# Kernel optimization log

Measured on AMD Instinct MI355X. Metric: run time of the kernel, lower is better.

Reference implementation:

```python
import jax, jax.numpy as jnp
import numpy as np

B, C, H, W = 4, 256, 48, 48
NUM_HEADS = 8
INTER = C // 2          # squeeze_ratio = 2
HEAD_DIM = INTER // NUM_HEADS


def setup_inputs() -> dict:
    key = jax.random.key(0)
    ks = jax.random.split(key, 11)
    s_in = 1.0 / np.sqrt(C)      # torch Conv2d default init scale (uniform bound)
    s_mid = 1.0 / np.sqrt(INTER)
    return {
        "rgb":   jax.random.normal(ks[0], (B, C, H, W), jnp.float32),
        "depth": jax.random.normal(ks[1], (B, C, H, W), jnp.float32),
        "rgbd":  jax.random.normal(ks[2], (B, C, H, W), jnp.float32),
        # 1x1 convs == channel matmuls; store as [out, in] plus bias
        "Wq": jax.random.uniform(ks[3], (INTER, C), jnp.float32, -s_in, s_in),
        "bq": jax.random.uniform(ks[4], (INTER,), jnp.float32, -s_in, s_in),
        "Wk": jax.random.uniform(ks[5], (INTER, C), jnp.float32, -s_in, s_in),
        "bk": jax.random.uniform(ks[6], (INTER,), jnp.float32, -s_in, s_in),
        "Wv": jax.random.uniform(ks[7], (INTER, C), jnp.float32, -s_in, s_in),
        "bv": jax.random.uniform(ks[8], (INTER,), jnp.float32, -s_in, s_in),
        "Wo": jax.random.uniform(ks[9], (C, INTER), jnp.float32, -s_mid, s_mid),
        "bo": jax.random.uniform(ks[10], (C,), jnp.float32, -s_mid, s_mid),
    }


def _proj(x, Wm, bm):
    # 1x1 conv: [B,Cin,H,W] -> [B,Cout,H,W]
    return jnp.einsum('oc,bchw->bohw', Wm, x) + bm[None, :, None, None]


def reference(rgb, depth, rgbd, Wq, bq, Wk, bk, Wv, bv, Wo, bo):
    P = H * W
    # project and split heads: [B, heads, head_dim, P]
    Q = _proj(rgb, Wq, bq).reshape(B, NUM_HEADS, HEAD_DIM, P)
    K = _proj(depth, Wk, bk).reshape(B, NUM_HEADS, HEAD_DIM, P)
    V = _proj(rgbd, Wv, bv).reshape(B, NUM_HEADS, HEAD_DIM, P)
    scale = 1.0 / np.sqrt(HEAD_DIM)
    # scores [B, heads, P(q), P(k)]
    scores = jnp.einsum('bhdq,bhdk->bhqk', Q, K) * scale
    attn = jax.nn.softmax(scores, axis=-1)
    # output [B, heads, head_dim, P(q)] -> [B, INTER, H, W]
    out = jnp.einsum('bhqk,bhdk->bhdq', attn, V).reshape(B, INTER, H, W)
    refined = _proj(out, Wo, bo)
    return (rgb + refined, depth + refined, rgbd + refined)
```

## Files before the change

kernel.cpp:

```cpp
#include <hip/hip_runtime.h>
#include <stdint.h>

#define P_TOT 2304
#define C_IN  256
#define INTER 128
#define NH    8
#define HD    16
#define QSCALE 0.36067376022224087f

typedef short sh4 __attribute__((ext_vector_type(4)));
typedef short sh8 __attribute__((ext_vector_type(8)));
typedef float fl4 __attribute__((ext_vector_type(4)));

static __device__ __forceinline__ unsigned short f2bf(float f) {
    union { float f; unsigned u; } v; v.f = f;
    return (unsigned short)((v.u + 0x7fffu + ((v.u >> 16) & 1u)) >> 16);
}
static __device__ __forceinline__ unsigned pack_bf2(float a, float b) {
    union { float f; unsigned u; } x, y; x.f = a; y.f = b;
    return __builtin_amdgcn_perm(y.u + 0x8000u, x.u + 0x8000u, 0x07060302u);
}
static __device__ __forceinline__ unsigned pack_bf2_trunc(float a, float b) {
    union { float f; unsigned u; } x, y; x.f = a; y.f = b;
    return __builtin_amdgcn_perm(y.u, x.u, 0x07060302u);
}

__global__ __launch_bounds__(256) void k_prep(
    const float* __restrict__ Wq, const float* __restrict__ Wk,
    const float* __restrict__ Wv, const float* __restrict__ Wo,
    unsigned short* __restrict__ Wb) {
    int i = blockIdx.x * 256 + threadIdx.x;
    int seg = i >> 15, off = i & 32767;
    const float* s = (seg == 0 ? Wq : (seg == 1 ? Wk : (seg == 2 ? Wv : Wo)));
    Wb[i] = f2bf(s[off]);
}

__global__ __launch_bounds__(256) void k_qkv(
    const float* __restrict__ rgb, const float* __restrict__ depth,
    const float* __restrict__ rgbd, const unsigned short* __restrict__ Wb,
    const float* __restrict__ bq, const float* __restrict__ bk,
    const float* __restrict__ bv,
    unsigned short* __restrict__ Qt, unsigned short* __restrict__ Kt,
    unsigned short* __restrict__ Vn) {
    __shared__ fl4 ldsA[2][8][64];
    int nt = blockIdx.x, pb = blockIdx.y;
    int pr = pb >> 2, b = pb & 3;
    const unsigned short* W = Wb + pr * (INTER * C_IN);
    const float* bias = (pr == 0 ? bq : (pr == 1 ? bk : bv));
    const float* X = (pr == 0 ? rgb : (pr == 1 ? depth : rgbd)) + (size_t)b * C_IN * P_TOT;
    int tid = threadIdx.x, w = tid >> 6, lane = tid & 63;
    int wp = w & 1, chalf = w >> 1;
    int l15 = lane & 15, quad = lane >> 4;
    int p = nt * 32 + wp * 16 + l15;
    fl4 zero = {0.f, 0.f, 0.f, 0.f};
    fl4 acc[8];
#pragma unroll
    for (int i = 0; i < 8; ++i) acc[i] = zero;
    const float* xcol = X + p;
    int kbeg = chalf * 128;
#pragma unroll
    for (int kk = 0; kk < 128; kk += 32) {
        int k0 = kbeg + kk;
        int cb = k0 + quad * 8;
        unsigned u[8];
#pragma unroll
        for (int j = 0; j < 8; ++j) {
            union { float f; unsigned uu; } t;
            t.f = xcol[(size_t)(cb + j) * P_TOT];
            u[j] = t.uu;
        }
        sh8 bfr;
        unsigned* bu = (unsigned*)&bfr;
        bu[0] = __builtin_amdgcn_perm(u[1] + 0x8000u, u[0] + 0x8000u, 0x07060302u);
        bu[1] = __builtin_amdgcn_perm(u[3] + 0x8000u, u[2] + 0x8000u, 0x07060302u);
        bu[2] = __builtin_amdgcn_perm(u[5] + 0x8000u, u[4] + 0x8000u, 0x07060302u);
        bu[3] = __builtin_amdgcn_perm(u[7] + 0x8000u, u[6] + 0x8000u, 0x07060302u);
        if (pr < 2) {
#pragma unroll
            for (int mf = 0; mf < 8; ++mf) {
                sh8 af = *(const sh8*)(W + (size_t)(mf * 16 + l15) * C_IN + k0 + quad * 8);
                acc[mf] = __builtin_amdgcn_mfma_f32_16x16x32_bf16(af, bfr, acc[mf], 0, 0, 0);
            }
        } else {
#pragma unroll
            for (int mf = 0; mf < 8; ++mf) {
                sh8 af = *(const sh8*)(W + (size_t)(mf * 16 + l15) * C_IN + k0 + quad * 8);
                acc[mf] = __builtin_amdgcn_mfma_f32_16x16x32_bf16(bfr, af, acc[mf], 0, 0, 0);
            }
        }
    }
    if (chalf == 1) {
#pragma unroll
        for (int mf = 0; mf < 8; ++mf) ldsA[wp][mf][lane] = acc[mf];
    }
    __syncthreads();
    if (chalf == 1) return;
#pragma unroll
    for (int mf = 0; mf < 8; ++mf) acc[mf] += ldsA[wp][mf][lane];
    if (pr < 2) {
        unsigned short* dst0 = (pr == 0 ? Qt : Kt);
        float sc = (pr == 0 ? QSCALE : 1.0f);
#pragma unroll
        for (int mf = 0; mf < 8; ++mf) {
            float4 bb = *(const float4*)(bias + mf * 16 + quad * 4);
            uint2 v;
            v.x = pack_bf2((acc[mf][0] + bb.x) * sc, (acc[mf][1] + bb.y) * sc);
            v.y = pack_bf2((acc[mf][2] + bb.z) * sc, (acc[mf][3] + bb.w) * sc);
            *(uint2*)(dst0 + ((size_t)(b * NH + mf) * P_TOT + p) * HD + quad * 4) = v;
        }
    } else {
        int pv = nt * 32 + wp * 16 + quad * 4;
#pragma unroll
        for (int mf = 0; mf < 8; ++mf) {
            float bb = bias[mf * 16 + l15];
            uint2 v;
            v.x = pack_bf2(acc[mf][0] + bb, acc[mf][1] + bb);
            v.y = pack_bf2(acc[mf][2] + bb, acc[mf][3] + bb);
            *(uint2*)(Vn + ((size_t)(b * NH + mf) * HD + l15) * P_TOT + pv) = v;
        }
    }
}

__global__ __launch_bounds__(256) void k_attn(
    const unsigned short* __restrict__ Qt, const unsigned short* __restrict__ Kt,
    const unsigned short* __restrict__ Vn, unsigned short* __restrict__ Ot) {
    __shared__ fl4 ldsO[4][3][64];
    __shared__ fl4 ldsL[3][64];
    int qt = blockIdx.x, h = blockIdx.y, b = blockIdx.z;
    int tid = threadIdx.x, w = tid >> 6, lane = tid & 63;
    int l15 = lane & 15, quad = lane >> 4;
    int bh = b * NH + h;
    int q0 = qt * 64 + l15;
    const unsigned short* qb = Qt + (size_t)bh * P_TOT * HD + quad * 4;
    sh4 qf0 = *(const sh4*)(qb + (size_t)q0 * HD);
    sh4 qf1 = *(const sh4*)(qb + (size_t)(q0 + 16) * HD);
    sh4 qf2 = *(const sh4*)(qb + (size_t)(q0 + 32) * HD);
    sh4 qf3 = *(const sh4*)(qb + (size_t)(q0 + 48) * HD);
    int ko = w * (P_TOT / 4);
    const unsigned short* kb = Kt + (size_t)bh * P_TOT * HD + (size_t)(ko + l15) * HD + quad * 4;
    const unsigned short* vb = Vn + ((size_t)bh * HD + l15) * P_TOT + quad * 4 + ko;
    fl4 zero = {0.f, 0.f, 0.f, 0.f};
    fl4 o0 = zero, o1 = zero, o2 = zero, o3 = zero;
    fl4 ls = zero;
    const int NIT = P_TOT / 4 / 16;
    sh4 kf = *(const sh4*)kb;
    sh4 vf = *(const sh4*)vb;
    for (int it = 0; it < NIT; ++it) {
        int nx = (it + 1 < NIT) ? it + 1 : it;
        sh4 kf_n = *(const sh4*)(kb + (size_t)nx * 16 * HD);
        sh4 vf_n = *(const sh4*)(vb + nx * 16);
        fl4 s0 = __builtin_amdgcn_mfma_f32_16x16x16bf16_1k(kf, qf0, zero, 0, 0, 0);
        fl4 s1 = __builtin_amdgcn_mfma_f32_16x16x16bf16_1k(kf, qf1, zero, 0, 0, 0);
        fl4 s2 = __builtin_amdgcn_mfma_f32_16x16x16bf16_1k(kf, qf2, zero, 0, 0, 0);
        fl4 s3 = __builtin_amdgcn_mfma_f32_16x16x16bf16_1k(kf, qf3, zero, 0, 0, 0);
        float e00 = __builtin_amdgcn_exp2f(s0[0]), e01 = __builtin_amdgcn_exp2f(s0[1]);
        float e02 = __builtin_amdgcn_exp2f(s0[2]), e03 = __builtin_amdgcn_exp2f(s0[3]);
        float e10 = __builtin_amdgcn_exp2f(s1[0]), e11 = __builtin_amdgcn_exp2f(s1[1]);
        float e12 = __builtin_amdgcn_exp2f(s1[2]), e13 = __builtin_amdgcn_exp2f(s1[3]);
        float e20 = __builtin_amdgcn_exp2f(s2[0]), e21 = __builtin_amdgcn_exp2f(s2[1]);
        float e22 = __builtin_amdgcn_exp2f(s2[2]), e23 = __builtin_amdgcn_exp2f(s2[3]);
        float e30 = __builtin_amdgcn_exp2f(s3[0]), e31 = __builtin_amdgcn_exp2f(s3[1]);
        float e32 = __builtin_amdgcn_exp2f(s3[2]), e33 = __builtin_amdgcn_exp2f(s3[3]);
        ls[0] += (e00 + e01) + (e02 + e03);
        ls[1] += (e10 + e11) + (e12 + e13);
        ls[2] += (e20 + e21) + (e22 + e23);
        ls[3] += (e30 + e31) + (e32 + e33);
        sh4 pf0, pf1, pf2, pf3;
        ((unsigned*)&pf0)[0] = pack_bf2_trunc(e00, e01);
        ((unsigned*)&pf0)[1] = pack_bf2_trunc(e02, e03);
        ((unsigned*)&pf1)[0] = pack_bf2_trunc(e10, e11);
        ((unsigned*)&pf1)[1] = pack_bf2_trunc(e12, e13);
        ((unsigned*)&pf2)[0] = pack_bf2_trunc(e20, e21);
        ((unsigned*)&pf2)[1] = pack_bf2_trunc(e22, e23);
        ((unsigned*)&pf3)[0] = pack_bf2_trunc(e30, e31);
        ((unsigned*)&pf3)[1] = pack_bf2_trunc(e32, e33);
        o0 = __builtin_amdgcn_mfma_f32_16x16x16bf16_1k(vf, pf0, o0, 0, 0, 0);
        o1 = __builtin_amdgcn_mfma_f32_16x16x16bf16_1k(vf, pf1, o1, 0, 0, 0);
        o2 = __builtin_amdgcn_mfma_f32_16x16x16bf16_1k(vf, pf2, o2, 0, 0, 0);
        o3 = __builtin_amdgcn_mfma_f32_16x16x16bf16_1k(vf, pf3, o3, 0, 0, 0);
        kf = kf_n;
        vf = vf_n;
    }
    if (w > 0) {
        ldsO[0][w - 1][lane] = o0;
        ldsO[1][w - 1][lane] = o1;
        ldsO[2][w - 1][lane] = o2;
        ldsO[3][w - 1][lane] = o3;
        ldsL[w - 1][lane] = ls;
    }
    __syncthreads();
    if (w > 0) return;
#pragma unroll
    for (int s = 0; s < 3; ++s) {
        o0 += ldsO[0][s][lane];
        o1 += ldsO[1][s][lane];
        o2 += ldsO[2][s][lane];
        o3 += ldsO[3][s][lane];
        ls += ldsL[s][lane];
    }
#pragma unroll
    for (int i = 0; i < 4; ++i) {
        ls[i] += __shfl_xor(ls[i], 16);
        ls[i] += __shfl_xor(ls[i], 32);
    }
    float i0 = 1.f / ls[0], i1 = 1.f / ls[1], i2 = 1.f / ls[2], i3 = 1.f / ls[3];
    unsigned short* ob = Ot + (size_t)bh * P_TOT * HD + quad * 4;
    uint2 v;
    v.x = pack_bf2(o0[0] * i0, o0[1] * i0); v.y = pack_bf2(o0[2] * i0, o0[3] * i0);
    *(uint2*)(ob + (size_t)q0 * HD) = v;
    v.x = pack_bf2(o1[0] * i1, o1[1] * i1); v.y = pack_bf2(o1[2] * i1, o1[3] * i1);
    *(uint2*)(ob + (size_t)(q0 + 16) * HD) = v;
    v.x = pack_bf2(o2[0] * i2, o2[1] * i2); v.y = pack_bf2(o2[2] * i2, o2[3] * i2);
    *(uint2*)(ob + (size_t)(q0 + 32) * HD) = v;
    v.x = pack_bf2(o3[0] * i3, o3[1] * i3); v.y = pack_bf2(o3[2] * i3, o3[3] * i3);
    *(uint2*)(ob + (size_t)(q0 + 48) * HD) = v;
}

__global__ __launch_bounds__(256) void k_out(
    const unsigned short* __restrict__ Ot, const unsigned short* __restrict__ Wob,
    const float* __restrict__ bo, const float* __restrict__ rgb,
    const float* __restrict__ depth, const float* __restrict__ rgbd,
    float* __restrict__ out) {
    int nt = blockIdx.x, mg = blockIdx.y, b = blockIdx.z;
    int tid = threadIdx.x, w = tid >> 6, lane = tid & 63;
    int l15 = lane & 15, quad = lane >> 4;
    int mf = mg * 4 + w;
    int p0 = nt * 16;
    fl4 zero = {0.f, 0.f, 0.f, 0.f};
    fl4 acc = zero;
#pragma unroll
    for (int k0 = 0; k0 < INTER; k0 += 32) {
        int h = (k0 >> 4) + (quad >> 1);
        int doff = 8 * (quad & 1);
        sh8 bfr = *(const sh8*)(Ot + ((size_t)(b * NH + h) * P_TOT + p0 + l15) * HD + doff);
        sh8 af = *(const sh8*)(Wob + (size_t)(mf * 16 + l15) * INTER + k0 + quad * 8);
        acc = __builtin_amdgcn_mfma_f32_16x16x32_bf16(bfr, af, acc, 0, 0, 0);
    }
    const size_t outsz = (size_t)4 * C_IN * P_TOT;
    int ch = mf * 16 + l15;
    float bb = bo[ch];
    size_t idx = ((size_t)b * C_IN + ch) * P_TOT + p0 + quad * 4;
    float r0 = acc[0] + bb, r1 = acc[1] + bb, r2 = acc[2] + bb, r3 = acc[3] + bb;
    float4 a = *(const float4*)(rgb + idx);
    float4 d = *(const float4*)(depth + idx);
    float4 g = *(const float4*)(rgbd + idx);
    float4 o;
    o.x = a.x + r0; o.y = a.y + r1; o.z = a.z + r2; o.w = a.w + r3;
    *(float4*)(out + idx) = o;
    o.x = d.x + r0; o.y = d.y + r1; o.z = d.z + r2; o.w = d.w + r3;
    *(float4*)(out + outsz + idx) = o;
    o.x = g.x + r0; o.y = g.y + r1; o.z = g.z + r2; o.w = g.w + r3;
    *(float4*)(out + 2 * outsz + idx) = o;
}

extern "C" void kernel_launch(void* const* d_in, const int* in_sizes, int n_in,
                              void* d_out, int out_size, void* d_ws, size_t ws_size,
                              hipStream_t stream) {
    (void)in_sizes; (void)n_in; (void)out_size; (void)ws_size;
    const float* rgb   = (const float*)d_in[0];
    const float* depth = (const float*)d_in[1];
    const float* rgbd  = (const float*)d_in[2];
    const float* Wq = (const float*)d_in[3];
    const float* bq = (const float*)d_in[4];
    const float* Wk = (const float*)d_in[5];
    const float* bk = (const float*)d_in[6];
    const float* Wv = (const float*)d_in[7];
    const float* bv = (const float*)d_in[8];
    const float* Wo = (const float*)d_in[9];
    const float* bo = (const float*)d_in[10];

    float* outp = (float*)d_out;
    unsigned short* Qt = (unsigned short*)d_out;
    unsigned short* Kt = Qt + (size_t)4 * P_TOT * INTER;
    unsigned short* Vn = Kt + (size_t)4 * P_TOT * INTER;
    unsigned short* Ot = (unsigned short*)d_ws;
    unsigned short* Wb = Ot + (size_t)4 * P_TOT * INTER;

    k_prep<<<512, 256, 0, stream>>>(Wq, Wk, Wv, Wo, Wb);
    k_qkv<<<dim3(72, 12), 256, 0, stream>>>(rgb, depth, rgbd, Wb, bq, bk, bv, Qt, Kt, Vn);
    k_attn<<<dim3(36, NH, 4), 256, 0, stream>>>(Qt, Kt, Vn, Ot);
    k_out<<<dim3(144, 4, 4), 256, 0, stream>>>(Ot, Wb + 3 * 32768, bo, rgb, depth, rgbd, outp);
}
```

Measured before the change: 170.0 us.

## Store Q/K/V in fragment-tiled layout and split keys across eight waves

Result: faster. 154.4 us (-9.2%).

```diff
diff --git a/kernel.cpp b/kernel.cpp
--- a/kernel.cpp
+++ b/kernel.cpp
@@ -6,6 +6,7 @@
 #define INTER 128
 #define NH    8
 #define HD    16
+#define NKB   144
 #define QSCALE 0.36067376022224087f
 
 typedef short sh4 __attribute__((ext_vector_type(4)));
@@ -97,6 +98,8 @@
     if (chalf == 1) return;
 #pragma unroll
     for (int mf = 0; mf < 8; ++mf) acc[mf] += ldsA[wp][mf][lane];
+    int tile = nt * 2 + wp;
+    int loff = (quad * 16 + l15) * 4;
     if (pr < 2) {
         unsigned short* dst0 = (pr == 0 ? Qt : Kt);
         float sc = (pr == 0 ? QSCALE : 1.0f);
@@ -106,49 +109,46 @@
             uint2 v;
             v.x = pack_bf2((acc[mf][0] + bb.x) * sc, (acc[mf][1] + bb.y) * sc);
             v.y = pack_bf2((acc[mf][2] + bb.z) * sc, (acc[mf][3] + bb.w) * sc);
-            *(uint2*)(dst0 + ((size_t)(b * NH + mf) * P_TOT + p) * HD + quad * 4) = v;
+            *(uint2*)(dst0 + (size_t)((b * NH + mf) * NKB + tile) * 256 + loff) = v;
         }
     } else {
-        int pv = nt * 32 + wp * 16 + quad * 4;
 #pragma unroll
         for (int mf = 0; mf < 8; ++mf) {
             float bb = bias[mf * 16 + l15];
             uint2 v;
             v.x = pack_bf2(acc[mf][0] + bb, acc[mf][1] + bb);
             v.y = pack_bf2(acc[mf][2] + bb, acc[mf][3] + bb);
-            *(uint2*)(Vn + ((size_t)(b * NH + mf) * HD + l15) * P_TOT + pv) = v;
-        }
-    }
-}
-
-__global__ __launch_bounds__(256) void k_attn(
+            *(uint2*)(Vn + (size_t)((b * NH + mf) * NKB + tile) * 256 + loff) = v;
+        }
+    }
+}
+
+__global__ __launch_bounds__(512) void k_attn(
     const unsigned short* __restrict__ Qt, const unsigned short* __restrict__ Kt,
     const unsigned short* __restrict__ Vn, unsigned short* __restrict__ Ot) {
-    __shared__ fl4 ldsO[4][3][64];
-    __shared__ fl4 ldsL[3][64];
+    __shared__ fl4 red[4][5][64];
     int qt = blockIdx.x, h = blockIdx.y, b = blockIdx.z;
     int tid = threadIdx.x, w = tid >> 6, lane = tid & 63;
     int l15 = lane & 15, quad = lane >> 4;
     int bh = b * NH + h;
-    int q0 = qt * 64 + l15;
-    const unsigned short* qb = Qt + (size_t)bh * P_TOT * HD + quad * 4;
-    sh4 qf0 = *(const sh4*)(qb + (size_t)q0 * HD);
-    sh4 qf1 = *(const sh4*)(qb + (size_t)(q0 + 16) * HD);
-    sh4 qf2 = *(const sh4*)(qb + (size_t)(q0 + 32) * HD);
-    sh4 qf3 = *(const sh4*)(qb + (size_t)(q0 + 48) * HD);
-    int ko = w * (P_TOT / 4);
-    const unsigned short* kb = Kt + (size_t)bh * P_TOT * HD + (size_t)(ko + l15) * HD + quad * 4;
-    const unsigned short* vb = Vn + ((size_t)bh * HD + l15) * P_TOT + quad * 4 + ko;
+    int loff = (quad * 16 + l15) * 4;
+    const unsigned short* qb = Qt + (size_t)(bh * NKB + qt * 4) * 256 + loff;
+    sh4 qf0 = *(const sh4*)(qb);
+    sh4 qf1 = *(const sh4*)(qb + 256);
+    sh4 qf2 = *(const sh4*)(qb + 512);
+    sh4 qf3 = *(const sh4*)(qb + 768);
+    const int NIT = NKB / 8;
+    const unsigned short* kb = Kt + (size_t)(bh * NKB + w * NIT) * 256 + loff;
+    const unsigned short* vb = Vn + (size_t)(bh * NKB + w * NIT) * 256 + loff;
     fl4 zero = {0.f, 0.f, 0.f, 0.f};
     fl4 o0 = zero, o1 = zero, o2 = zero, o3 = zero;
     fl4 ls = zero;
-    const int NIT = P_TOT / 4 / 16;
     sh4 kf = *(const sh4*)kb;
     sh4 vf = *(const sh4*)vb;
     for (int it = 0; it < NIT; ++it) {
         int nx = (it + 1 < NIT) ? it + 1 : it;
-        sh4 kf_n = *(const sh4*)(kb + (size_t)nx * 16 * HD);
-        sh4 vf_n = *(const sh4*)(vb + nx * 16);
+        sh4 kf_n = *(const sh4*)(kb + (size_t)nx * 256);
+        sh4 vf_n = *(const sh4*)(vb + (size_t)nx * 256);
         fl4 s0 = __builtin_amdgcn_mfma_f32_16x16x16bf16_1k(kf, qf0, zero, 0, 0, 0);
         fl4 s1 = __builtin_amdgcn_mfma_f32_16x16x16bf16_1k(kf, qf1, zero, 0, 0, 0);
         fl4 s2 = __builtin_amdgcn_mfma_f32_16x16x16bf16_1k(kf, qf2, zero, 0, 0, 0);
@@ -181,29 +181,33 @@
         kf = kf_n;
         vf = vf_n;
     }
-    if (w > 0) {
-        ldsO[0][w - 1][lane] = o0;
-        ldsO[1][w - 1][lane] = o1;
-        ldsO[2][w - 1][lane] = o2;
-        ldsO[3][w - 1][lane] = o3;
-        ldsL[w - 1][lane] = ls;
-    }
-    __syncthreads();
-    if (w > 0) return;
-#pragma unroll
-    for (int s = 0; s < 3; ++s) {
-        o0 += ldsO[0][s][lane];
-        o1 += ldsO[1][s][lane];
-        o2 += ldsO[2][s][lane];
-        o3 += ldsO[3][s][lane];
-        ls += ldsL[s][lane];
-    }
+#pragma unroll
+    for (int step = 4; step >= 1; step >>= 1) {
+        if (w >= step && w < 2 * step) {
+            red[w - step][0][lane] = o0;
+            red[w - step][1][lane] = o1;
+            red[w - step][2][lane] = o2;
+            red[w - step][3][lane] = o3;
+            red[w - step][4][lane] = ls;
+        }
+        __syncthreads();
+        if (w < step) {
+            o0 += red[w][0][lane];
+            o1 += red[w][1][lane];
+            o2 += red[w][2][lane];
+            o3 += red[w][3][lane];
+            ls += red[w][4][lane];
+        }
+        __syncthreads();
+    }
+    if (w != 0) return;
 #pragma unroll
     for (int i = 0; i < 4; ++i) {
         ls[i] += __shfl_xor(ls[i], 16);
         ls[i] += __shfl_xor(ls[i], 32);
     }
     float i0 = 1.f / ls[0], i1 = 1.f / ls[1], i2 = 1.f / ls[2], i3 = 1.f / ls[3];
+    int q0 = qt * 64 + l15;
     unsigned short* ob = Ot + (size_t)bh * P_TOT * HD + quad * 4;
     uint2 v;
     v.x = pack_bf2(o0[0] * i0, o0[1] * i0); v.y = pack_bf2(o0[2] * i0, o0[3] * i0);
@@ -278,6 +282,6 @@
 
     k_prep<<<512, 256, 0, stream>>>(Wq, Wk, Wv, Wo, Wb);
     k_qkv<<<dim3(72, 12), 256, 0, stream>>>(rgb, depth, rgbd, Wb, bq, bk, bv, Qt, Kt, Vn);
-    k_attn<<<dim3(36, NH, 4), 256, 0, stream>>>(Qt, Kt, Vn, Ot);
+    k_attn<<<dim3(36, NH, 4), 512, 0, stream>>>(Qt, Kt, Vn, Ot);
     k_out<<<dim3(144, 4, 4), 256, 0, stream>>>(Ot, Wb + 3 * 32768, bo, rgb, depth, rgbd, outp);
 }
```
